# Kernel tuning notes

Hardware: AMD Instinct MI355X
Metric: run time of the kernel (lower is better)

The kernel has to match this reference:

```python
import jax, jax.numpy as jnp
import numpy as np

N = 1024
H = 256
W = 256
TILE = 16
FX = 300.0
FY = 300.0
CX = 128.0
CY = 128.0
NEAR = 0.1
FAR = 100.0
FRUSTUM_R = 1.0      # cfg.frustum_culling_radius
TILE_CULL_R = 3.0    # cfg.tile_culling_radius (bcircle path)
T_THRESH = 1e-4      # cfg.T_thresh
N_TH = H // TILE
N_TW = W // TILE


def quat_to_rot(q):
    # q: [N,4] (w,x,y,z), normalized inside
    q = q / jnp.linalg.norm(q, axis=-1, keepdims=True)
    w, x, y, z = q[:, 0], q[:, 1], q[:, 2], q[:, 3]
    r0 = jnp.stack([1 - 2 * (y * y + z * z), 2 * (x * y - w * z), 2 * (x * z + w * y)], -1)
    r1 = jnp.stack([2 * (x * y + w * z), 1 - 2 * (x * x + z * z), 2 * (y * z - w * x)], -1)
    r2 = jnp.stack([2 * (x * z - w * y), 2 * (y * z + w * x), 1 - 2 * (x * x + y * y)], -1)
    return jnp.stack([r0, r1, r2], axis=1)  # [N,3,3]


def setup_inputs() -> dict:
    key = jax.random.key(0)
    ks = jax.random.split(key, 6)
    # place gaussians inside the view frustum: depth 2..6, normalized xy in +-0.4
    nxy = jax.random.uniform(ks[0], (N, 2), minval=-0.4, maxval=0.4, dtype=jnp.float32)
    z = jax.random.uniform(ks[1], (N, 1), minval=2.0, maxval=6.0, dtype=jnp.float32)
    mean = jnp.concatenate([nxy * z, z], axis=1)  # [N,3]
    qvec = jax.random.normal(ks[2], (N, 4), dtype=jnp.float32)
    log_svec = jnp.float32(np.log(0.02)) + 0.3 * jax.random.normal(ks[3], (N, 3), dtype=jnp.float32)
    color = jax.random.uniform(ks[4], (N, 3), dtype=jnp.float32)
    alpha = 2.0 * jax.random.normal(ks[5], (N,), dtype=jnp.float32)
    c2w = jnp.concatenate([jnp.eye(3, dtype=jnp.float32), jnp.zeros((3, 1), jnp.float32)], axis=1)
    return {"mean": mean, "qvec": qvec, "log_svec": log_svec, "color": color, "alpha": alpha, "c2w": c2w}


def reference(mean, qvec, log_svec, color, alpha, c2w):
    svec = jnp.exp(log_svec)                      # [N,3]
    a = jax.nn.sigmoid(alpha)                     # [N]
    Rcw = c2w[:, :3]                              # camera->world rotation (cols x,y,z)
    t = c2w[:, 3]
    # world -> camera: p_cam = Rcw^T (p - t) == (p - t) @ Rcw
    mean_cam = (mean - t) @ Rcw                   # [N,3]
    depth = mean_cam[:, 2]
    zc = jnp.maximum(depth, 1e-6)
    inv_z = 1.0 / zc
    x, y = mean_cam[:, 0], mean_cam[:, 1]
    mx, my = x * inv_z, y * inv_z                 # 2D mean in camera-plane units
    # projection Jacobian J [N,2,3]
    zero = jnp.zeros_like(inv_z)
    J = jnp.stack([jnp.stack([inv_z, zero, -x * inv_z * inv_z], -1),
                   jnp.stack([zero, inv_z, -y * inv_z * inv_z], -1)], axis=1)
    Rq = quat_to_rot(qvec)                        # [N,3,3]
    cov3d = jnp.einsum('nij,nj,nkj->nik', Rq, svec * svec, Rq)
    JW = jnp.einsum('nij,kj->nik', J, Rcw)        # J @ Rcw^T (world->cam rot)
    cov = jnp.einsum('nij,njk,nlk->nil', JW, cov3d, JW)  # [N,2,2]
    cov = (cov + jnp.swapaxes(cov, -1, -2)) / 2.0
    c00, c01, c11 = cov[:, 0, 0], cov[:, 0, 1], cov[:, 1, 1]
    m = (c00 + c11) / 2.0
    det = c00 * c11 - c01 * c01
    radius = jax.lax.stop_gradient(jnp.sqrt(m + jnp.sqrt(jnp.clip(m * m - det, 0.0))))
    # --- frustum culling (no-grad boolean mask, bounding-sphere style) ---
    r3d = FRUSTUM_R * jnp.max(svec, axis=-1)
    half_w = (W / 2.0) / FX
    half_h = (H / 2.0) / FY
    marg = r3d * inv_z
    maskf = ((depth > NEAR) & (depth < FAR) &
             (jnp.abs(mx) < half_w + marg) & (jnp.abs(my) < half_h + marg))
    maskf = jax.lax.stop_gradient(maskf)
    # --- per-tile bcircle culling mask ---
    psx, psy = 1.0 / FX, 1.0 / FY
    tlx, tly = -CX / FX, -CY / FY
    tx0 = tlx + jnp.arange(N_TW, dtype=jnp.float32) * TILE * psx
    tx1 = tx0 + TILE * psx
    ty0 = tly + jnp.arange(N_TH, dtype=jnp.float32) * TILE * psy
    ty1 = ty0 + TILE * psy
    smx, smy = jax.lax.stop_gradient(mx), jax.lax.stop_gradient(my)
    dxt = jnp.maximum(jnp.maximum(tx0[None, :] - smx[:, None], smx[:, None] - tx1[None, :]), 0.0)  # [N,ntw]
    dyt = jnp.maximum(jnp.maximum(ty0[None, :] - smy[:, None], smy[:, None] - ty1[None, :]), 0.0)  # [N,nth]
    r2 = (radius * TILE_CULL_R) ** 2
    tmask = (dxt[:, None, :] ** 2 + dyt[:, :, None] ** 2) <= r2[:, None, None]  # [N,nth,ntw]
    tmask = jnp.repeat(jnp.repeat(tmask, TILE, axis=1), TILE, axis=2)           # [N,H,W]
    # --- per-pixel gaussian weights ---
    detc = jnp.maximum(det, 1e-12)
    ia, ib, ic = c11 / detc, -c01 / detc, c00 / detc   # inverse 2x2 cov
    px = tlx + (jnp.arange(W, dtype=jnp.float32) + 0.5) * psx
    py = tly + (jnp.arange(H, dtype=jnp.float32) + 0.5) * psy
    dx = px[None, :] - mx[:, None]                 # [N,W]
    dy = py[None, :] - my[:, None]                 # [N,H]
    quad = (ia[:, None, None] * (dx * dx)[:, None, :]
            + 2.0 * ib[:, None, None] * dy[:, :, None] * dx[:, None, :]
            + ic[:, None, None] * (dy * dy)[:, :, None])      # [N,H,W]
    G = jnp.exp(-0.5 * quad)
    w = a[:, None, None] * G * maskf[:, None, None].astype(G.dtype) * tmask.astype(G.dtype)
    # --- global depth sort (per-tile order == global order restricted to tile) ---
    skey = jnp.where(maskf, jax.lax.stop_gradient(depth), jnp.float32(1e10))
    order = jnp.argsort(skey)
    w = w[order]
    color_s = color[order]
    # --- front-to-back alpha compositing with early-termination mask ---
    Tcum = jnp.cumprod(1.0 - w, axis=0)
    Tprev = jnp.concatenate([jnp.ones((1, H, W), w.dtype), Tcum[:-1]], axis=0)
    weight = jnp.where(Tprev > T_THRESH, Tprev * w, 0.0)
    out = jnp.einsum('nhw,nc->hwc', weight, color_s)   # [H,W,3]
    return out
```

## Files before the change

### kernel.cpp

```cpp
#include <hip/hip_runtime.h>
#include <hip/hip_bf16.h>
#include <math.h>

#define GN      1024
#define GH      256
#define GW      256
#define GTILE   16
#define N_TW    (GW / GTILE)
#define N_TH    (GH / GTILE)
#define FXc     300.0f
#define FYc     300.0f
#define CXc     128.0f
#define CYc     128.0f
#define NEARc   0.1f
#define FARc    100.0f
#define T_TH    0.0001f
#define PSX     (1.0f / FXc)
#define PSY     (1.0f / FYc)
#define TLX     (-CXc / FXc)
#define TLY     (-CYc / FYc)
#define HALF_W  (GW * 0.5f / FXc)
#define HALF_H  (GH * 0.5f / FYc)

__global__ __launch_bounds__(256) void splat_all(
    const float* __restrict__ mean, const float* __restrict__ qvec,
    const float* __restrict__ lsv,  const float* __restrict__ color,
    const float* __restrict__ alpha, const float* __restrict__ c2w,
    float* __restrict__ out)
{
    __shared__ float  S1x[GN], S1y[GN], S1d[GN];
    __shared__ int    S1i[GN];
    __shared__ float  skey[GN];
    __shared__ float4 uP0[GN];
    __shared__ float4 uP1[GN];
    __shared__ float  uP2[GN];
    __shared__ int    sord[GN];
    __shared__ int    scnt[16];
    __shared__ int    sbase;

    const int tid  = threadIdx.x;
    const int lane = tid & 63;
    const int wv   = tid >> 6;

    float R[3][3], t[3];
#pragma unroll
    for (int r = 0; r < 3; ++r) {
        R[r][0] = c2w[r * 4 + 0];
        R[r][1] = c2w[r * 4 + 1];
        R[r][2] = c2w[r * 4 + 2];
        t[r]    = c2w[r * 4 + 3];
    }

    const float tx0 = TLX + (float)blockIdx.x * (GTILE * PSX);
    const float tx1 = tx0 + GTILE * PSX;
    const float ty0 = TLY + (float)blockIdx.y * (GTILE * PSY);
    const float ty1 = ty0 + GTILE * PSY;

    float s_xc[4], s_yc[4], s_dep[4];
    bool  s_keep[4];

#pragma unroll
    for (int c = 0; c < 4; ++c) {
        const int i = c * 256 + tid;
        const float m0 = mean[i * 3 + 0] - t[0];
        const float m1 = mean[i * 3 + 1] - t[1];
        const float m2 = mean[i * 3 + 2] - t[2];
        const float l0 = lsv[i * 3 + 0];
        const float l1 = lsv[i * 3 + 1];
        const float l2 = lsv[i * 3 + 2];

        const float xc    = m0 * R[0][0] + m1 * R[1][0] + m2 * R[2][0];
        const float yc    = m0 * R[0][1] + m1 * R[1][1] + m2 * R[2][1];
        const float depth = m0 * R[0][2] + m1 * R[1][2] + m2 * R[2][2];

        const float zc = fmaxf(depth, 1e-6f);
        const float iz = 1.0f / zc;
        const float mx = xc * iz, my = yc * iz;

        const float s0 = __expf(l0);
        const float s1 = __expf(l1);
        const float s2 = __expf(l2);
        const float r3d  = fmaxf(s0, fmaxf(s1, s2));
        const float marg = r3d * iz;
        const bool maskf = (depth > NEARc) && (depth < FARc) &&
                           (fabsf(mx) < HALF_W + marg) && (fabsf(my) < HALF_H + marg);

        const float rb2 = 9.45f * r3d * r3d * iz * iz * (2.0f + mx * mx + my * my);

        const float dxt = fmaxf(fmaxf(tx0 - mx, mx - tx1), 0.0f);
        const float dyt = fmaxf(fmaxf(ty0 - my, my - ty1), 0.0f);

        s_xc[c] = xc; s_yc[c] = yc; s_dep[c] = depth;
        s_keep[c] = maskf && (dxt * dxt + dyt * dyt <= rb2);
    }

    unsigned long long bm[4];
#pragma unroll
    for (int c = 0; c < 4; ++c) {
        bm[c] = __ballot(s_keep[c]);
        if (lane == 0) scnt[c * 4 + wv] = __popcll(bm[c]);
    }
    __syncthreads();

    int cnt[16];
#pragma unroll
    for (int k = 0; k < 16; ++k) cnt[k] = scnt[k];
    int chunkbase[5];
    chunkbase[0] = 0;
#pragma unroll
    for (int c = 0; c < 4; ++c)
        chunkbase[c + 1] = chunkbase[c] + cnt[c * 4 + 0] + cnt[c * 4 + 1] +
                           cnt[c * 4 + 2] + cnt[c * 4 + 3];
    const int n1 = chunkbase[4];

#pragma unroll
    for (int c = 0; c < 4; ++c) {
        if (s_keep[c]) {
            int off = chunkbase[c];
            for (int w2 = 0; w2 < wv; ++w2) off += cnt[c * 4 + w2];
            off += __popcll(bm[c] & ((1ull << lane) - 1ull));
            S1x[off] = s_xc[c];
            S1y[off] = s_yc[c];
            S1d[off] = s_dep[c];
            S1i[off] = c * 256 + tid;
        }
    }
    if (tid == 0) sbase = 0;
    __syncthreads();

    for (int base = 0; base < n1; base += 256) {
        const int tt = base + tid;
        bool keep2 = false;
        float depth = 0.f, mx = 0.f, my = 0.f, ia = 0.f, ib = 0.f, ic = 0.f;
        float aa = 0.f, cr0 = 0.f, cg0 = 0.f, cb0 = 0.f;
        if (tt < n1) {
            const float xc = S1x[tt];
            const float yc = S1y[tt];
            depth = S1d[tt];
            const int idx = S1i[tt];

            const float zc = fmaxf(depth, 1e-6f);
            const float iz = 1.0f / zc;
            mx = xc * iz; my = yc * iz;

            const float4 q4 = ((const float4*)qvec)[idx];
            const float l0 = lsv[idx * 3 + 0];
            const float l1 = lsv[idx * 3 + 1];
            const float l2 = lsv[idx * 3 + 2];
            const float al = alpha[idx];
            cr0 = color[idx * 3 + 0];
            cg0 = color[idx * 3 + 1];
            cb0 = color[idx * 3 + 2];

            float qw = q4.x, qx = q4.y, qy = q4.z, qz = q4.w;
            const float qinv = 1.0f / sqrtf(qw * qw + qx * qx + qy * qy + qz * qz);
            qw *= qinv; qx *= qinv; qy *= qinv; qz *= qinv;
            float Rq[3][3];
            Rq[0][0] = 1.0f - 2.0f * (qy * qy + qz * qz);
            Rq[0][1] = 2.0f * (qx * qy - qw * qz);
            Rq[0][2] = 2.0f * (qx * qz + qw * qy);
            Rq[1][0] = 2.0f * (qx * qy + qw * qz);
            Rq[1][1] = 1.0f - 2.0f * (qx * qx + qz * qz);
            Rq[1][2] = 2.0f * (qy * qz - qw * qx);
            Rq[2][0] = 2.0f * (qx * qz - qw * qy);
            Rq[2][1] = 2.0f * (qy * qz + qw * qx);
            Rq[2][2] = 1.0f - 2.0f * (qx * qx + qy * qy);

            const float s0 = __expf(l0);
            const float s1 = __expf(l1);
            const float s2 = __expf(l2);
            const float v0 = s0 * s0, v1 = s1 * s1, v2 = s2 * s2;

            float V[3][3];
#pragma unroll
            for (int a = 0; a < 3; ++a)
#pragma unroll
                for (int b = 0; b < 3; ++b)
                    V[a][b] = Rq[a][0] * v0 * Rq[b][0] + Rq[a][1] * v1 * Rq[b][1] +
                              Rq[a][2] * v2 * Rq[b][2];

            float J[2][3];
            J[0][0] = iz;   J[0][1] = 0.0f; J[0][2] = -xc * iz * iz;
            J[1][0] = 0.0f; J[1][1] = iz;   J[1][2] = -yc * iz * iz;

            float JW[2][3];
#pragma unroll
            for (int r = 0; r < 2; ++r)
#pragma unroll
                for (int k = 0; k < 3; ++k)
                    JW[r][k] = J[r][0] * R[k][0] + J[r][1] * R[k][1] + J[r][2] * R[k][2];

            float M[2][3];
#pragma unroll
            for (int r = 0; r < 2; ++r)
#pragma unroll
                for (int cc = 0; cc < 3; ++cc)
                    M[r][cc] = JW[r][0] * V[0][cc] + JW[r][1] * V[1][cc] + JW[r][2] * V[2][cc];
            const float cov00 = M[0][0] * JW[0][0] + M[0][1] * JW[0][1] + M[0][2] * JW[0][2];
            const float cov01 = M[0][0] * JW[1][0] + M[0][1] * JW[1][1] + M[0][2] * JW[1][2];
            const float cov10 = M[1][0] * JW[0][0] + M[1][1] * JW[0][1] + M[1][2] * JW[0][2];
            const float cov11 = M[1][0] * JW[1][0] + M[1][1] * JW[1][1] + M[1][2] * JW[1][2];

            const float c00 = cov00;
            const float c01 = 0.5f * (cov01 + cov10);
            const float c11 = cov11;

            const float mm  = 0.5f * (c00 + c11);
            const float det = c00 * c11 - c01 * c01;
            const float radius = sqrtf(mm + sqrtf(fmaxf(mm * mm - det, 0.0f)));

            const float r3d  = fmaxf(s0, fmaxf(s1, s2));
            const float marg = r3d * iz;
            const bool maskf = (depth > NEARc) && (depth < FARc) &&
                               (fabsf(mx) < HALF_W + marg) && (fabsf(my) < HALF_H + marg);

            const float detc = fmaxf(det, 1e-12f);
            const float idet = 1.0f / detc;
            ia =  c11 * idet;
            ib = -c01 * idet;
            ic =  c00 * idet;

            const float sg = 1.0f / (1.0f + __expf(-al));
            aa = maskf ? sg : 0.0f;
            const float rr = radius * 3.0f;
            const float r2 = rr * rr;

            const float dxt = fmaxf(fmaxf(tx0 - mx, mx - tx1), 0.0f);
            const float dyt = fmaxf(fmaxf(ty0 - my, my - ty1), 0.0f);
            keep2 = (aa > 0.0f) && (dxt * dxt + dyt * dyt <= r2);
        }

        const unsigned long long b2 = __ballot(keep2);
        if (lane == 0) scnt[wv] = __popcll(b2);
        __syncthreads();
        int off = sbase;
        for (int w2 = 0; w2 < wv; ++w2) off += scnt[w2];
        const int chunk_total = scnt[0] + scnt[1] + scnt[2] + scnt[3];
        if (keep2) {
            const int p = off + __popcll(b2 & ((1ull << lane) - 1ull));
            skey[p] = depth;
            uP0[p]  = make_float4(mx, my, ia, ib);
            uP1[p]  = make_float4(ic, aa, cr0, cg0);
            uP2[p]  = cb0;
        }
        __syncthreads();
        if (tid == 0) sbase += chunk_total;
        __syncthreads();
    }
    const int n2 = sbase;

    for (int tt = tid; tt < n2; tt += 256) {
        const float k = skey[tt];
        int rank = 0;
        for (int j = 0; j < n2; ++j) {
            const float kj = skey[j];
            rank += (kj < k) || (kj == k && j < tt);
        }
        sord[rank] = tt;
    }
    __syncthreads();

    const int tx = tid & 15;
    const int ty = tid >> 4;
    const int wp = blockIdx.x * GTILE + tx;
    const int hp = blockIdx.y * GTILE + ty;
    const float px = TLX + ((float)wp + 0.5f) * PSX;
    const float py = TLY + ((float)hp + 0.5f) * PSY;

    float T = 1.0f, cr = 0.0f, cg = 0.0f, cb = 0.0f;

    for (int s = 0; s < n2; ++s) {
        if (s && (s & 63) == 0) {
            if (__syncthreads_and(T <= T_TH)) break;
        }
        const int p = sord[s];
        const float4 p0 = uP0[p];
        const float4 p1 = uP1[p];
        const float cbv = uP2[p];
        const float dx = px - p0.x, dy = py - p0.y;
        const float quad = p0.z * dx * dx + 2.0f * p0.w * dx * dy + p1.x * dy * dy;
        const float G = __expf(-0.5f * quad);
        const float w = p1.y * G;
        const float wt = (T > T_TH) ? T * w : 0.0f;
        cr += wt * p1.z;
        cg += wt * p1.w;
        cb += wt * cbv;
        T *= (1.0f - w);
    }

    const int o = (hp * GW + wp) * 3;
    out[o + 0] = cr;
    out[o + 1] = cg;
    out[o + 2] = cb;
}

extern "C" void kernel_launch(void* const* d_in, const int* in_sizes, int n_in,
                              void* d_out, int out_size, void* d_ws, size_t ws_size,
                              hipStream_t stream) {
    const float* mean  = (const float*)d_in[0];
    const float* qvec  = (const float*)d_in[1];
    const float* lsv   = (const float*)d_in[2];
    const float* color = (const float*)d_in[3];
    const float* alpha = (const float*)d_in[4];
    const float* c2w   = (const float*)d_in[5];
    float* out = (float*)d_out;

    hipLaunchKernelGGL(splat_all, dim3(N_TW, N_TH), dim3(256), 0, stream,
                       mean, qvec, lsv, color, alpha, c2w, out);
}
```

Measured before the change: 13.48 us.

## Use 512-thread blocks for culling and sort, drop early-exit barrier in compositing

Result: faster. 11.62 us (-13.8%).

```diff
diff --git a/kernel.cpp b/kernel.cpp
--- a/kernel.cpp
+++ b/kernel.cpp
@@ -22,7 +22,9 @@
 #define HALF_W  (GW * 0.5f / FXc)
 #define HALF_H  (GH * 0.5f / FYc)
 
-__global__ __launch_bounds__(256) void splat_all(
+#define NT      512
+
+__global__ __launch_bounds__(NT) void splat_all(
     const float* __restrict__ mean, const float* __restrict__ qvec,
     const float* __restrict__ lsv,  const float* __restrict__ color,
     const float* __restrict__ alpha, const float* __restrict__ c2w,
@@ -36,7 +38,6 @@
     __shared__ float  uP2[GN];
     __shared__ int    sord[GN];
     __shared__ int    scnt[16];
-    __shared__ int    sbase;
 
     const int tid  = threadIdx.x;
     const int lane = tid & 63;
@@ -56,12 +57,12 @@
     const float ty0 = TLY + (float)blockIdx.y * (GTILE * PSY);
     const float ty1 = ty0 + GTILE * PSY;
 
-    float s_xc[4], s_yc[4], s_dep[4];
-    bool  s_keep[4];
-
-#pragma unroll
-    for (int c = 0; c < 4; ++c) {
-        const int i = c * 256 + tid;
+    float s_xc[2], s_yc[2], s_dep[2];
+    bool  s_keep[2];
+
+#pragma unroll
+    for (int c = 0; c < 2; ++c) {
+        const int i = c * NT + tid;
         const float m0 = mean[i * 3 + 0] - t[0];
         const float m1 = mean[i * 3 + 1] - t[1];
         const float m2 = mean[i * 3 + 2] - t[2];
@@ -77,10 +78,7 @@
         const float iz = 1.0f / zc;
         const float mx = xc * iz, my = yc * iz;
 
-        const float s0 = __expf(l0);
-        const float s1 = __expf(l1);
-        const float s2 = __expf(l2);
-        const float r3d  = fmaxf(s0, fmaxf(s1, s2));
+        const float r3d  = __expf(fmaxf(l0, fmaxf(l1, l2)));
         const float marg = r3d * iz;
         const bool maskf = (depth > NEARc) && (depth < FARc) &&
                            (fabsf(mx) < HALF_W + marg) && (fabsf(my) < HALF_H + marg);
@@ -94,41 +92,44 @@
         s_keep[c] = maskf && (dxt * dxt + dyt * dyt <= rb2);
     }
 
-    unsigned long long bm[4];
-#pragma unroll
-    for (int c = 0; c < 4; ++c) {
+    unsigned long long bm[2];
+#pragma unroll
+    for (int c = 0; c < 2; ++c) {
         bm[c] = __ballot(s_keep[c]);
-        if (lane == 0) scnt[c * 4 + wv] = __popcll(bm[c]);
+        if (lane == 0) scnt[c * 8 + wv] = __popcll(bm[c]);
     }
     __syncthreads();
 
     int cnt[16];
 #pragma unroll
     for (int k = 0; k < 16; ++k) cnt[k] = scnt[k];
-    int chunkbase[5];
+    int chunkbase[3];
     chunkbase[0] = 0;
 #pragma unroll
-    for (int c = 0; c < 4; ++c)
-        chunkbase[c + 1] = chunkbase[c] + cnt[c * 4 + 0] + cnt[c * 4 + 1] +
-                           cnt[c * 4 + 2] + cnt[c * 4 + 3];
-    const int n1 = chunkbase[4];
-
-#pragma unroll
-    for (int c = 0; c < 4; ++c) {
+    for (int c = 0; c < 2; ++c) {
+        int s = 0;
+#pragma unroll
+        for (int w2 = 0; w2 < 8; ++w2) s += cnt[c * 8 + w2];
+        chunkbase[c + 1] = chunkbase[c] + s;
+    }
+    const int n1 = chunkbase[2];
+
+#pragma unroll
+    for (int c = 0; c < 2; ++c) {
         if (s_keep[c]) {
             int off = chunkbase[c];
-            for (int w2 = 0; w2 < wv; ++w2) off += cnt[c * 4 + w2];
+            for (int w2 = 0; w2 < wv; ++w2) off += cnt[c * 8 + w2];
             off += __popcll(bm[c] & ((1ull << lane) - 1ull));
             S1x[off] = s_xc[c];
             S1y[off] = s_yc[c];
             S1d[off] = s_dep[c];
-            S1i[off] = c * 256 + tid;
-        }
-    }
-    if (tid == 0) sbase = 0;
+            S1i[off] = c * NT + tid;
+        }
+    }
     __syncthreads();
 
-    for (int base = 0; base < n1; base += 256) {
+    int s2base = 0;
+    for (int base = 0; base < n1; base += NT) {
         const int tt = base + tid;
         bool keep2 = false;
         float depth = 0.f, mx = 0.f, my = 0.f, ia = 0.f, ib = 0.f, ic = 0.f;
@@ -233,9 +234,11 @@
         const unsigned long long b2 = __ballot(keep2);
         if (lane == 0) scnt[wv] = __popcll(b2);
         __syncthreads();
-        int off = sbase;
+        int off = s2base;
         for (int w2 = 0; w2 < wv; ++w2) off += scnt[w2];
-        const int chunk_total = scnt[0] + scnt[1] + scnt[2] + scnt[3];
+        int ctot = 0;
+#pragma unroll
+        for (int w2 = 0; w2 < 8; ++w2) ctot += scnt[w2];
         if (keep2) {
             const int p = off + __popcll(b2 & ((1ull << lane) - 1ull));
             skey[p] = depth;
@@ -243,13 +246,12 @@
             uP1[p]  = make_float4(ic, aa, cr0, cg0);
             uP2[p]  = cb0;
         }
+        s2base += ctot;
         __syncthreads();
-        if (tid == 0) sbase += chunk_total;
-        __syncthreads();
-    }
-    const int n2 = sbase;
-
-    for (int tt = tid; tt < n2; tt += 256) {
+    }
+    const int n2 = s2base;
+
+    for (int tt = tid; tt < n2; tt += NT) {
         const float k = skey[tt];
         int rank = 0;
         for (int j = 0; j < n2; ++j) {
@@ -260,38 +262,37 @@
     }
     __syncthreads();
 
-    const int tx = tid & 15;
-    const int ty = tid >> 4;
-    const int wp = blockIdx.x * GTILE + tx;
-    const int hp = blockIdx.y * GTILE + ty;
-    const float px = TLX + ((float)wp + 0.5f) * PSX;
-    const float py = TLY + ((float)hp + 0.5f) * PSY;
-
-    float T = 1.0f, cr = 0.0f, cg = 0.0f, cb = 0.0f;
-
-    for (int s = 0; s < n2; ++s) {
-        if (s && (s & 63) == 0) {
-            if (__syncthreads_and(T <= T_TH)) break;
-        }
-        const int p = sord[s];
-        const float4 p0 = uP0[p];
-        const float4 p1 = uP1[p];
-        const float cbv = uP2[p];
-        const float dx = px - p0.x, dy = py - p0.y;
-        const float quad = p0.z * dx * dx + 2.0f * p0.w * dx * dy + p1.x * dy * dy;
-        const float G = __expf(-0.5f * quad);
-        const float w = p1.y * G;
-        const float wt = (T > T_TH) ? T * w : 0.0f;
-        cr += wt * p1.z;
-        cg += wt * p1.w;
-        cb += wt * cbv;
-        T *= (1.0f - w);
-    }
-
-    const int o = (hp * GW + wp) * 3;
-    out[o + 0] = cr;
-    out[o + 1] = cg;
-    out[o + 2] = cb;
+    if (tid < 256) {
+        const int tx = tid & 15;
+        const int ty = tid >> 4;
+        const int wp = blockIdx.x * GTILE + tx;
+        const int hp = blockIdx.y * GTILE + ty;
+        const float px = TLX + ((float)wp + 0.5f) * PSX;
+        const float py = TLY + ((float)hp + 0.5f) * PSY;
+
+        float T = 1.0f, cr = 0.0f, cg = 0.0f, cb = 0.0f;
+
+        for (int s = 0; s < n2; ++s) {
+            const int p = sord[s];
+            const float4 p0 = uP0[p];
+            const float4 p1 = uP1[p];
+            const float cbv = uP2[p];
+            const float dx = px - p0.x, dy = py - p0.y;
+            const float quad = p0.z * dx * dx + 2.0f * p0.w * dx * dy + p1.x * dy * dy;
+            const float G = __expf(-0.5f * quad);
+            const float w = p1.y * G;
+            const float wt = (T > T_TH) ? T * w : 0.0f;
+            cr += wt * p1.z;
+            cg += wt * p1.w;
+            cb += wt * cbv;
+            T *= (1.0f - w);
+        }
+
+        const int o = (hp * GW + wp) * 3;
+        out[o + 0] = cr;
+        out[o + 1] = cg;
+        out[o + 2] = cb;
+    }
 }
 
 extern "C" void kernel_launch(void* const* d_in, const int* in_sizes, int n_in,
@@ -305,6 +306,6 @@
     const float* c2w   = (const float*)d_in[5];
     float* out = (float*)d_out;
 
-    hipLaunchKernelGGL(splat_all, dim3(N_TW, N_TH), dim3(256), 0, stream,
+    hipLaunchKernelGGL(splat_all, dim3(N_TW, N_TH), dim3(NT), 0, stream,
                        mean, qvec, lsv, color, alpha, c2w, out);
 }
```
